# Performance work log

Hardware: AMD Instinct MI355X
Metric: run time of the kernel (lower is better)

The kernel has to match this reference:

```python
import jax, jax.numpy as jnp
import numpy as np
from jax import lax

NPOINT = 1024
K = 32
EPS = 1e-5  # BatchNorm eps (torch default)


def farthest_point_sample(xyz, npoint):
    # xyz: [B, N, 3] -> [B, npoint] int32 indices.
    # Deterministic variant: initial farthest point fixed to index 0
    # (original uses torch.randint; fixed seed point for reproducibility).
    B, N, _ = xyz.shape

    def step(carry, _):
        distance, farthest = carry  # [B,N], [B]
        centroid = jnp.take_along_axis(xyz, farthest[:, None, None], axis=1)  # [B,1,3]
        d = jnp.sum((xyz - centroid) ** 2, axis=-1)  # [B,N]
        distance = jnp.minimum(distance, d)
        new_far = jnp.argmax(distance, axis=-1).astype(jnp.int32)
        return (distance, new_far), farthest

    init = (jnp.full((B, N), 1e10, dtype=xyz.dtype), jnp.zeros((B,), jnp.int32))
    _, cents = lax.scan(step, init, None, length=npoint)  # [npoint, B]
    return cents.T  # [B, npoint]


def _gather_points(p, i):
    # p: [N, C], i: [S, K] -> [S, K, C]
    return p[i]


gather = jax.vmap(_gather_points)


def _mlp_layer(x, W, b, g, bt):
    # x: [B, Cin, K, S]; 1x1 Conv2d + BatchNorm2d (training stats) + ReLU
    y = jnp.einsum('bckn,oc->bokn', x, W) + b[None, :, None, None]
    m = y.mean(axis=(0, 2, 3), keepdims=True)
    v = y.var(axis=(0, 2, 3), keepdims=True)  # biased var, as torch BN training
    y = g[None, :, None, None] * (y - m) * lax.rsqrt(v + EPS) + bt[None, :, None, None]
    return jax.nn.relu(y)


def setup_inputs() -> dict:
    key = jax.random.key(0)
    ks = jax.random.split(key, 10)
    B, N, D = 16, 4096, 64
    xyz = jax.random.normal(ks[0], (B, N, 3), dtype=jnp.float32)
    points = jax.random.normal(ks[1], (B, N, D), dtype=jnp.float32)
    cin = 3 + D
    mlp = [64, 64, 128]
    params = {}
    last = cin
    for li, cout in enumerate(mlp):
        kw = jax.random.fold_in(ks[2], li)
        params[f'W{li+1}'] = jax.random.normal(kw, (cout, last), dtype=jnp.float32) * (1.0 / np.sqrt(last))
        params[f'b{li+1}'] = jnp.zeros((cout,), jnp.float32)
        params[f'g{li+1}'] = jnp.ones((cout,), jnp.float32)
        params[f'bt{li+1}'] = jnp.zeros((cout,), jnp.float32)
        last = cout
    return {'xyz': xyz, 'points': points, **params}


def reference(xyz, points, W1, b1, g1, bt1, W2, b2, g2, bt2, W3, b3, g3, bt3):
    # --- sample_and_group ---
    fidx = farthest_point_sample(xyz, NPOINT)                       # [B,S]
    new_xyz = jnp.take_along_axis(xyz, fidx[:, :, None], axis=1)    # [B,S,3]
    # pairwise squared distance centroids -> all points: [B,S,N]
    dist = jnp.sum((new_xyz[:, :, None, :] - xyz[:, None, :, :]) ** 2, axis=-1)
    _, idx = lax.top_k(-dist, K)                                    # k nearest, [B,S,K]
    grouped_xyz = gather(xyz, idx)                                  # [B,S,K,3]
    grouped_xyz_norm = grouped_xyz - new_xyz[:, :, None, :]
    grouped_pts = gather(points, idx)                               # [B,S,K,D]
    new_points = jnp.concatenate([grouped_xyz_norm, grouped_pts], axis=-1)  # [B,S,K,C]
    # --- pointwise MLP + max pool over neighbors ---
    x = jnp.transpose(new_points, (0, 3, 2, 1))                     # [B,C,K,S]
    x = _mlp_layer(x, W1, b1, g1, bt1)
    x = _mlp_layer(x, W2, b2, g2, bt2)
    x = _mlp_layer(x, W3, b3, g3, bt3)
    out = jnp.max(x, axis=2)                                        # [B,128,S]
    return (new_xyz, out)
```

## Files before the change

### kernel.cpp

```cpp
#include <hip/hip_runtime.h>
#include <hip/hip_bf16.h>

typedef __attribute__((ext_vector_type(8))) unsigned short u16x8;
typedef __attribute__((ext_vector_type(8))) short bf16x8;
typedef __attribute__((ext_vector_type(4))) float f32x4;

#define DEVI __device__ __forceinline__

constexpr int Bc = 16;
constexpr int Nc = 4096;
constexpr int Sc = 1024;
constexpr int Kc = 32;
constexpr int Dc = 64;
constexpr int C1 = 67;
constexpr int Mtot = Bc * Sc * Kc;
constexpr float EPSc = 1e-5f;
constexpr float CNTinv = 1.0f / (float)Mtot;
constexpr int NREP = 8;
constexpr int REPSTRIDE = 512;

DEVI float sqdist3(float dx, float dy, float dz) {
  return __fadd_rn(__fadd_rn(__fmul_rn(dx, dx), __fmul_rn(dy, dy)), __fmul_rn(dz, dz));
}
DEVI unsigned long long umax64(unsigned long long a, unsigned long long b) { return a > b ? a : b; }
DEVI float bf2f(unsigned short u) { return __uint_as_float(((unsigned)u) << 16); }
DEVI unsigned short f2bf(float f) {
  __hip_bfloat16 h = __float2bfloat16(f);
  unsigned short u;
  __builtin_memcpy(&u, &h, 2);
  return u;
}
DEVI unsigned pack_bf2(float a, float b) {
  return (unsigned)f2bf(a) | ((unsigned)f2bf(b) << 16);
}

#define DPP_STAGE(v, OP, CTRL, MASK)                                                       \
  {                                                                                        \
    int _t = __builtin_amdgcn_update_dpp(__float_as_int(v), __float_as_int(v), CTRL, MASK, \
                                         0xF, false);                                      \
    v = OP(v, __int_as_float(_t));                                                         \
  }
DEVI float wave_fmax63(float v) {
  DPP_STAGE(v, fmaxf, 0xB1, 0xF)
  DPP_STAGE(v, fmaxf, 0x4E, 0xF)
  DPP_STAGE(v, fmaxf, 0x141, 0xF)
  DPP_STAGE(v, fmaxf, 0x140, 0xF)
  DPP_STAGE(v, fmaxf, 0x142, 0xA)
  DPP_STAGE(v, fmaxf, 0x143, 0xC)
  return __int_as_float(__builtin_amdgcn_readlane(__float_as_int(v), 63));
}
DEVI float wave_fmin63(float v) {
  DPP_STAGE(v, fminf, 0xB1, 0xF)
  DPP_STAGE(v, fminf, 0x4E, 0xF)
  DPP_STAGE(v, fminf, 0x141, 0xF)
  DPP_STAGE(v, fminf, 0x140, 0xF)
  DPP_STAGE(v, fminf, 0x142, 0xA)
  DPP_STAGE(v, fminf, 0x143, 0xC)
  return __int_as_float(__builtin_amdgcn_readlane(__float_as_int(v), 63));
}
#define DPP_STAGE_U(v, CTRL, MASK)                                                      \
  {                                                                                     \
    unsigned _t = (unsigned)__builtin_amdgcn_update_dpp((int)(v), (int)(v), CTRL, MASK, \
                                                        0xF, false);                    \
    v = (_t < v) ? _t : v;                                                              \
  }
DEVI unsigned wave_umin63(unsigned v) {
  DPP_STAGE_U(v, 0xB1, 0xF)
  DPP_STAGE_U(v, 0x4E, 0xF)
  DPP_STAGE_U(v, 0x141, 0xF)
  DPP_STAGE_U(v, 0x140, 0xF)
  DPP_STAGE_U(v, 0x142, 0xA)
  DPP_STAGE_U(v, 0x143, 0xC)
  return (unsigned)__builtin_amdgcn_readlane((int)v, 63);
}

__global__ __launch_bounds__(256) void fps_kernel(const float* __restrict__ xyz,
                                                  int* __restrict__ fidx) {
  __shared__ float4 lsc[Nc];
  __shared__ __align__(16) unsigned long long wkey[2][4];
  __shared__ int sidx[Sc];
  const int b = blockIdx.x;
  const float* xb = xyz + (size_t)b * Nc * 3;
  const int tid = threadIdx.x;
  const int lane = tid & 63, w = tid >> 6;

  float px[16], py[16], pz[16], dist[16];
#pragma unroll
  for (int i = 0; i < 16; ++i) {
    int p = tid + i * 256;
    px[i] = xb[p * 3 + 0];
    py[i] = xb[p * 3 + 1];
    pz[i] = xb[p * 3 + 2];
    dist[i] = 1e10f;
  }
  for (int e = tid; e < Nc; e += 256)
    lsc[e] = make_float4(xb[e * 3 + 0], xb[e * 3 + 1], xb[e * 3 + 2], 0.f);
  if (tid == 0) sidx[0] = 0;
  __syncthreads();

  int widx = 0;
  for (int t = 1; t < Sc; ++t) {
    const float4 c = lsc[widx];
    float nd[16];
#pragma unroll
    for (int i = 0; i < 16; ++i) {
      float d = sqdist3(px[i] - c.x, py[i] - c.y, pz[i] - c.z);
      float v = fminf(dist[i], d);
      dist[i] = v;
      nd[i] = v;
    }
    float t8[8], t4[4];
#pragma unroll
    for (int u = 0; u < 8; ++u) t8[u] = fmaxf(nd[u], nd[u + 8]);
#pragma unroll
    for (int u = 0; u < 4; ++u) t4[u] = fmaxf(t8[u], t8[u + 4]);
    const float mymax = fmaxf(fmaxf(t4[0], t4[1]), fmaxf(t4[2], t4[3]));
    const float maxw = wave_fmax63(mymax);
    unsigned lp = 0xFFFFFFFFu;
#pragma unroll
    for (int i = 15; i >= 0; --i) lp = (nd[i] == maxw) ? (unsigned)(tid + (i << 8)) : lp;
    const unsigned long long mask = __ballot(mymax == maxw);
    unsigned wavep;
    if (__builtin_popcountll(mask) == 1) {
      wavep = (unsigned)__builtin_amdgcn_readlane((int)lp, (int)__builtin_ctzll(mask));
    } else {
      wavep = wave_umin63(lp);
    }
    if (lane == 0)
      wkey[t & 1][w] = ((unsigned long long)__float_as_uint(maxw) << 32) |
                       (unsigned long long)(0xFFFFFFFFu - wavep);
    __syncthreads();
    const ulonglong2* wp = (const ulonglong2*)wkey[t & 1];
    ulonglong2 a0 = wp[0], a1 = wp[1];
    unsigned long long m = umax64(umax64(a0.x, a0.y), umax64(a1.x, a1.y));
    widx = (int)(0xFFFFFFFFu - (unsigned)(m & 0xFFFFFFFFu));
    if (tid == 0) sidx[t] = widx;
  }
  __syncthreads();
  for (int e = tid; e < Sc; e += 256) fidx[b * Sc + e] = sidx[e];
}

__global__ __launch_bounds__(256) void knn_kernel(const float* __restrict__ xyz,
                                                  const int* __restrict__ fidx,
                                                  float* __restrict__ new_xyz,
                                                  int* __restrict__ idx) {
  const int w = threadIdx.x >> 6;
  const int lane = threadIdx.x & 63;
  const int q = blockIdx.x * 4 + w;
  const int b = q >> 10;
  const int s = q & (Sc - 1);
  const float* xb = xyz + (size_t)b * Nc * 3;
  const int ci = fidx[b * Sc + s];
  const float cx = xb[ci * 3 + 0], cy = xb[ci * 3 + 1], cz = xb[ci * 3 + 2];
  if (lane == 0) {
    new_xyz[(b * Sc + s) * 3 + 0] = cx;
    new_xyz[(b * Sc + s) * 3 + 1] = cy;
    new_xyz[(b * Sc + s) * 3 + 2] = cz;
  }
  const float INF = __int_as_float(0x7F800000);
  const float* pp = xb + lane * 3;
  float d0 = INF, d1 = INF;
  int i0 = 0, i1 = 0;
#pragma unroll 4
  for (int i = 0; i < 64; ++i) {
    const float x = pp[i * 192 + 0], y = pp[i * 192 + 1], z = pp[i * 192 + 2];
    const float d = sqdist3(x - cx, y - cy, z - cz);
    const bool c0 = d < d0, c1 = d < d1;
    d1 = c0 ? d0 : (c1 ? d : d1);
    i1 = c0 ? i0 : (c1 ? i : i1);
    d0 = c0 ? d : d0;
    i0 = c0 ? i : i0;
  }
  unsigned long long taken = 0ull;
  int* outp = idx + ((size_t)b * Sc + s) * Kc;
#pragma unroll 1
  for (int r = 0; r < Kc; ++r) {
    const float mind = wave_fmin63(d0);
    const unsigned myp = (unsigned)(lane + (i0 << 6));
    const unsigned long long mask = __ballot(d0 == mind);
    unsigned W;
    if (__builtin_popcountll(mask) == 1) {
      W = (unsigned)__builtin_amdgcn_readlane((int)myp, (int)__builtin_ctzll(mask));
    } else {
      unsigned c = (d0 == mind) ? myp : 0xFFFFFFFFu;
      W = wave_umin63(c);
    }
    if (lane == 0) outp[r] = (int)W;
    if (myp == W) {
      taken |= (1ull << i0);
      d0 = d1;
      i0 = i1;
      d1 = INF;
      if (__float_as_uint(d0) == 0x7F800000u) {
        float e0 = INF, e1 = INF;
        int j0 = 0, j1 = 0;
#pragma unroll 4
        for (int i = 0; i < 64; ++i) {
          const float x = pp[i * 192 + 0], y = pp[i * 192 + 1], z = pp[i * 192 + 2];
          float d = sqdist3(x - cx, y - cy, z - cz);
          d = ((taken >> i) & 1ull) ? INF : d;
          const bool c0b = d < e0, c1b = d < e1;
          e1 = c0b ? e0 : (c1b ? d : e1);
          j1 = c0b ? j0 : (c1b ? i : j1);
          e0 = c0b ? d : e0;
          j0 = c0b ? i : j0;
        }
        d0 = e0; i0 = j0; d1 = e1; i1 = j1;
      }
    }
  }
}

__global__ __launch_bounds__(256) void conv1_kernel(
    const float* __restrict__ xyz, const float* __restrict__ points,
    const float* __restrict__ new_xyz, const int* __restrict__ idx,
    const float* __restrict__ W1, const float* __restrict__ b1,
    __hip_bfloat16* __restrict__ x1, float* __restrict__ statsOut) {
  __shared__ float feats[C1][68];
  __shared__ float Wt[C1][64];
  __shared__ float red1[4][16][8];
  const int tid = threadIdx.x;
  const int lane = tid & 63, w = tid >> 6;
  const int m0 = blockIdx.x * 64;
  for (int e = tid; e < 64 * C1; e += 256) {
    int c = e / C1, j = e % C1;
    Wt[j][c] = W1[e];
  }
  {
    const int p = tid >> 2, qd = tid & 3;
    const int m = m0 + p;
    const int b = m >> 15;
    const int s = (m >> 5) & (Sc - 1);
    const int i = idx[m];
    const float* pr = points + ((size_t)b * Nc + i) * Dc + qd * 16;
    float4 v0 = *(const float4*)(pr + 0);
    float4 v1 = *(const float4*)(pr + 4);
    float4 v2 = *(const float4*)(pr + 8);
    float4 v3 = *(const float4*)(pr + 12);
    float vv[16] = {v0.x, v0.y, v0.z, v0.w, v1.x, v1.y, v1.z, v1.w,
                    v2.x, v2.y, v2.z, v2.w, v3.x, v3.y, v3.z, v3.w};
    const int j0 = 3 + qd * 16;
#pragma unroll
    for (int u = 0; u < 16; ++u) feats[j0 + u][p] = vv[u];
    if (qd == 0) {
      const float* xp = xyz + ((size_t)b * Nc + i) * 3;
      const float* cp = new_xyz + ((size_t)b * Sc + s) * 3;
      feats[0][p] = xp[0] - cp[0];
      feats[1][p] = xp[1] - cp[1];
      feats[2][p] = xp[2] - cp[2];
    }
  }
  __syncthreads();
  const int c0 = (tid & 15) * 4, p0 = (tid >> 4) * 4;
  float acc[4][4];
#pragma unroll
  for (int cc = 0; cc < 4; ++cc) {
    float bb = b1[c0 + cc];
#pragma unroll
    for (int pp = 0; pp < 4; ++pp) acc[pp][cc] = bb;
  }
#pragma unroll 4
  for (int j = 0; j < C1; ++j) {
    const float4 f = *(const float4*)&feats[j][p0];
    const float4 wv = *(const float4*)&Wt[j][c0];
    const float fa[4] = {f.x, f.y, f.z, f.w};
    const float wa[4] = {wv.x, wv.y, wv.z, wv.w};
#pragma unroll
    for (int pp = 0; pp < 4; ++pp)
#pragma unroll
      for (int cc = 0; cc < 4; ++cc) acc[pp][cc] = fmaf(fa[pp], wa[cc], acc[pp][cc]);
  }
  float s_[4] = {0.f, 0.f, 0.f, 0.f}, q_[4] = {0.f, 0.f, 0.f, 0.f};
#pragma unroll
  for (int pp = 0; pp < 4; ++pp) {
    unsigned short hv[4];
#pragma unroll
    for (int cc = 0; cc < 4; ++cc) {
      hv[cc] = f2bf(acc[pp][cc]);
      float fr = bf2f(hv[cc]);
      s_[cc] += fr;
      q_[cc] += fr * fr;
    }
    unsigned r0 = (unsigned)hv[0] | ((unsigned)hv[1] << 16);
    unsigned r1 = (unsigned)hv[2] | ((unsigned)hv[3] << 16);
    unsigned short* dst = (unsigned short*)x1 + (size_t)(m0 + p0 + pp) * 64 + c0;
    *(uint2*)dst = make_uint2(r0, r1);
  }
#pragma unroll
  for (int cc = 0; cc < 4; ++cc) {
    s_[cc] += __shfl_xor(s_[cc], 16, 64);
    s_[cc] += __shfl_xor(s_[cc], 32, 64);
    q_[cc] += __shfl_xor(q_[cc], 16, 64);
    q_[cc] += __shfl_xor(q_[cc], 32, 64);
  }
  if (lane < 16) {
#pragma unroll
    for (int cc = 0; cc < 4; ++cc) {
      red1[w][lane][cc] = s_[cc];
      red1[w][lane][4 + cc] = q_[cc];
    }
  }
  __syncthreads();
  if (tid < 128) {
    int h = tid >> 6, ch = tid & 63;
    int g = ch >> 2, cc = ch & 3;
    float v = red1[0][g][h * 4 + cc] + red1[1][g][h * 4 + cc] + red1[2][g][h * 4 + cc] +
              red1[3][g][h * 4 + cc];
    atomicAdd(&statsOut[(blockIdx.x & (NREP - 1)) * REPSTRIDE + h * 64 + ch], v);
  }
}

template <int COUT, bool LAST>
__global__ __launch_bounds__(256) void convm_kernel(
    const __hip_bfloat16* __restrict__ xin, const float* __restrict__ statsIn,
    const float* __restrict__ gamma, const float* __restrict__ beta,
    const float* __restrict__ W, const float* __restrict__ bias,
    float* __restrict__ statsOut, __hip_bfloat16* __restrict__ xout,
    unsigned* __restrict__ ymm) {
  constexpr int NT = COUT / 16;
  __shared__ __align__(16) unsigned short fA[64 * 64];
  __shared__ __align__(16) unsigned short fW[COUT * 64];
  __shared__ float scs[64], shs[64];
  __shared__ float red[4][COUT][2];
  __shared__ float redmm[LAST ? 4 : 1][COUT][2];
  __shared__ unsigned short fStage[64][72];
  const int tid = threadIdx.x;
  const int lane = tid & 63, w = tid >> 6;
  const long m0 = (long)blockIdx.x * 64;

  if (tid < 64) {
    float s0 = 0.f, s1 = 0.f;
#pragma unroll
    for (int r = 0; r < NREP; ++r) {
      s0 += statsIn[r * REPSTRIDE + tid];
      s1 += statsIn[r * REPSTRIDE + 64 + tid];
    }
    float mean = s0 * CNTinv;
    float var = s1 * CNTinv - mean * mean;
    float sc = gamma[tid] * rsqrtf(var + EPSc);
    scs[tid] = sc;
    shs[tid] = beta[tid] - mean * sc;
  }
  for (int e = tid; e < COUT * 64; e += 256) {
    int r = e >> 6, k = e & 63;
    int byte = (k * 2) ^ ((r & 7) << 4);
    fW[r * 64 + (byte >> 1)] = f2bf(W[e]);
  }
  __syncthreads();
  {
    const int row = tid >> 2, cb = tid & 3;
    const unsigned short* src = (const unsigned short*)xin + (m0 + row) * 64 + cb * 16;
    u16x8 a = *(const u16x8*)src;
    u16x8 bv = *(const u16x8*)(src + 8);
    unsigned short o[16];
#pragma unroll
    for (int u = 0; u < 8; ++u) {
      int ch = cb * 16 + u;
      o[u] = f2bf(fmaxf(fmaf(scs[ch], bf2f(a[u]), shs[ch]), 0.f));
    }
#pragma unroll
    for (int u = 0; u < 8; ++u) {
      int ch = cb * 16 + 8 + u;
      o[8 + u] = f2bf(fmaxf(fmaf(scs[ch], bf2f(bv[u]), shs[ch]), 0.f));
    }
    int sw = (row & 7) << 4;
    *(bf16x8*)((char*)fA + row * 128 + ((cb * 32) ^ sw)) = *(bf16x8*)&o[0];
    *(bf16x8*)((char*)fA + row * 128 + ((cb * 32 + 16) ^ sw)) = *(bf16x8*)&o[8];
  }
  __syncthreads();

  const int fr = lane & 15, kchunk = lane >> 4;
  f32x4 acc[NT];
#pragma unroll
  for (int nt = 0; nt < NT; ++nt) {
    float bb = bias[nt * 16 + fr];
    acc[nt] = f32x4{bb, bb, bb, bb};
  }
  bf16x8 af0, af1;
  {
    int row = w * 16 + fr;
    int sw = (row & 7) << 4;
    af0 = *(bf16x8*)((char*)fA + row * 128 + ((kchunk * 16) ^ sw));
    af1 = *(bf16x8*)((char*)fA + row * 128 + ((64 + kchunk * 16) ^ sw));
  }
#pragma unroll
  for (int nt = 0; nt < NT; ++nt) {
    int r2 = nt * 16 + fr;
    int sw = (r2 & 7) << 4;
    bf16x8 bf0 = *(bf16x8*)((char*)fW + r2 * 128 + ((kchunk * 16) ^ sw));
    bf16x8 bf1 = *(bf16x8*)((char*)fW + r2 * 128 + ((64 + kchunk * 16) ^ sw));
    acc[nt] = __builtin_amdgcn_mfma_f32_16x16x32_bf16(af0, bf0, acc[nt], 0, 0, 0);
    acc[nt] = __builtin_amdgcn_mfma_f32_16x16x32_bf16(af1, bf1, acc[nt], 0, 0, 0);
  }

  float s_[NT], q_[NT], mn_[NT], mx_[NT];
#pragma unroll
  for (int nt = 0; nt < NT; ++nt) {
    s_[nt] = 0.f;
    q_[nt] = 0.f;
    mn_[nt] = 1e30f;
    mx_[nt] = -1e30f;
    unsigned short hv[4];
#pragma unroll
    for (int r = 0; r < 4; ++r) {
      hv[r] = f2bf(acc[nt][r]);
      float fr2 = bf2f(hv[r]);
      s_[nt] += fr2;
      q_[nt] += fr2 * fr2;
      if constexpr (LAST) {
        mn_[nt] = fminf(mn_[nt], fr2);
        mx_[nt] = fmaxf(mx_[nt], fr2);
      }
    }
    if constexpr (!LAST) {
#pragma unroll
      for (int r = 0; r < 4; ++r) fStage[w * 16 + kchunk * 4 + r][nt * 16 + fr] = hv[r];
    }
  }
#pragma unroll
  for (int nt = 0; nt < NT; ++nt) {
    s_[nt] += __shfl_xor(s_[nt], 16, 64);
    s_[nt] += __shfl_xor(s_[nt], 32, 64);
    q_[nt] += __shfl_xor(q_[nt], 16, 64);
    q_[nt] += __shfl_xor(q_[nt], 32, 64);
    if constexpr (LAST) {
      mn_[nt] = fminf(mn_[nt], __shfl_xor(mn_[nt], 16, 64));
      mn_[nt] = fminf(mn_[nt], __shfl_xor(mn_[nt], 32, 64));
      mx_[nt] = fmaxf(mx_[nt], __shfl_xor(mx_[nt], 16, 64));
      mx_[nt] = fmaxf(mx_[nt], __shfl_xor(mx_[nt], 32, 64));
    }
  }
  if (lane < 16) {
#pragma unroll
    for (int nt = 0; nt < NT; ++nt) {
      red[w][nt * 16 + lane][0] = s_[nt];
      red[w][nt * 16 + lane][1] = q_[nt];
      if constexpr (LAST) {
        redmm[w][nt * 16 + lane][0] = mn_[nt];
        redmm[w][nt * 16 + lane][1] = mx_[nt];
      }
    }
  }
  __syncthreads();
  if (tid < 2 * COUT) {
    int ch = tid >> 1, h = tid & 1;
    float v = red[0][ch][h] + red[1][ch][h] + red[2][ch][h] + red[3][ch][h];
    atomicAdd(&statsOut[(blockIdx.x & (NREP - 1)) * REPSTRIDE + h * COUT + ch], v);
  }
  if constexpr (LAST) {
    int sg = tid >> 7, ch = tid & 127;
    float mn = fminf(redmm[sg * 2][ch][0], redmm[sg * 2 + 1][ch][0]);
    float mx = fmaxf(redmm[sg * 2][ch][1], redmm[sg * 2 + 1][ch][1]);
    ymm[(size_t)(m0 / 32 + sg) * 128 + ch] = pack_bf2(mn, mx);
  } else {
    int row = tid >> 2, cb = tid & 3;
    unsigned short* dst = (unsigned short*)xout + (m0 + row) * 64 + cb * 16;
    *(uint4*)dst = *(uint4*)&fStage[row][cb * 16];
    *(uint4*)(dst + 8) = *(uint4*)&fStage[row][cb * 16 + 8];
  }
}

__global__ __launch_bounds__(256) void pool_kernel(const unsigned* __restrict__ ymm,
                                                   const float* __restrict__ stats,
                                                   const float* __restrict__ gamma,
                                                   const float* __restrict__ beta,
                                                   float* __restrict__ out) {
  __shared__ float sc[128], sh[128];
  __shared__ float res[128][33];
  const int tid = threadIdx.x;
  if (tid < 128) {
    float s0 = 0.f, s1 = 0.f;
#pragma unroll
    for (int r = 0; r < NREP; ++r) {
      s0 += stats[r * REPSTRIDE + tid];
      s1 += stats[r * REPSTRIDE + 128 + tid];
    }
    float mean = s0 * CNTinv;
    float var = s1 * CNTinv - mean * mean;
    float s = gamma[tid] * rsqrtf(var + EPSc);
    sc[tid] = s;
    sh[tid] = beta[tid] - mean * s;
  }
  __syncthreads();
  const int b = blockIdx.x >> 5;
  const int s0 = (blockIdx.x & 31) * 32;
  const int w = tid >> 6, lane = tid & 63;
  const int c0 = lane * 2;
  const float sc0 = sc[c0], sh0 = sh[c0], sc1 = sc[c0 + 1], sh1 = sh[c0 + 1];
  for (int si = 0; si < 8; ++si) {
    const int s = s0 + w * 8 + si;
    uint2 v = *(const uint2*)&ymm[(size_t)(b * Sc + s) * 128 + c0];
    float f0 = (sc0 >= 0.f) ? bf2f((unsigned short)(v.x >> 16)) : bf2f((unsigned short)(v.x & 0xFFFFu));
    float f1 = (sc1 >= 0.f) ? bf2f((unsigned short)(v.y >> 16)) : bf2f((unsigned short)(v.y & 0xFFFFu));
    res[c0][s - s0] = fmaxf(fmaf(sc0, f0, sh0), 0.f);
    res[c0 + 1][s - s0] = fmaxf(fmaf(sc1, f1, sh1), 0.f);
  }
  __syncthreads();
  const int c = tid >> 1, h = tid & 1;
  float* ob = out + (size_t)b * 128 * Sc + (size_t)c * Sc + s0 + h * 16;
#pragma unroll
  for (int u = 0; u < 16; ++u) ob[u] = res[c][h * 16 + u];
}

extern "C" void kernel_launch(void* const* d_in, const int* in_sizes, int n_in,
                              void* d_out, int out_size, void* d_ws, size_t ws_size,
                              hipStream_t stream) {
  const float* xyz = (const float*)d_in[0];
  const float* points = (const float*)d_in[1];
  const float* W1 = (const float*)d_in[2];
  const float* b1 = (const float*)d_in[3];
  const float* g1 = (const float*)d_in[4];
  const float* bt1 = (const float*)d_in[5];
  const float* W2 = (const float*)d_in[6];
  const float* b2 = (const float*)d_in[7];
  const float* g2 = (const float*)d_in[8];
  const float* bt2 = (const float*)d_in[9];
  const float* W3 = (const float*)d_in[10];
  const float* b3 = (const float*)d_in[11];
  const float* g3 = (const float*)d_in[12];
  const float* bt3 = (const float*)d_in[13];
  float* out = (float*)d_out;

  char* ws = (char*)d_ws;
  int* fidx = (int*)(ws + 0);
  int* idx = (int*)(ws + 65536);
  float* stats = (float*)(ws + 2162688);
  __hip_bfloat16* x1 = (__hip_bfloat16*)(ws + 2162688 + 16384);
  __hip_bfloat16* x2 = (__hip_bfloat16*)(ws + 2162688 + 16384 + 67108864);
  unsigned* ymm = (unsigned*)(ws + 2162688 + 16384 + 134217728);

  hipMemsetAsync(stats, 0, NREP * REPSTRIDE * sizeof(float), stream);
  fps_kernel<<<Bc, 256, 0, stream>>>(xyz, fidx);
  knn_kernel<<<Bc * Sc / 4, 256, 0, stream>>>(xyz, fidx, out, idx);
  conv1_kernel<<<Mtot / 64, 256, 0, stream>>>(xyz, points, out, idx, W1, b1, x1, stats);
  convm_kernel<64, false><<<Mtot / 64, 256, 0, stream>>>(x1, stats, g1, bt1, W2, b2,
                                                         stats + 128, x2, nullptr);
  convm_kernel<128, true><<<Mtot / 64, 256, 0, stream>>>(x2, stats + 128, g2, bt2, W3, b3,
                                                         stats + 256, nullptr, ymm);
  pool_kernel<<<Bc * (Sc / 32), 256, 0, stream>>>(ymm, stats + 256, g3, bt3,
                                                  out + Bc * Sc * 3);
}
```

Before: 1.168 ms.

## Use packed 64-bit key argmax in FPS and keep top-4 per lane in KNN

In the farthest-point-sampling loop, each point's distance and inverted index are packed into one 64-bit key, so a single max reduction (per thread, then a DPP wave reduction on lo/hi halves) replaces the float max, ballot, tie-break min and readlane sequence. This shortens the serial per-iteration dependency chain at the cost of more 64-bit compares. In the KNN kernel, each lane now keeps its 4 nearest candidates instead of 2, so the costly rescan of its 64 points is needed less often during the 32 extraction rounds. The price is more select instructions per point and more registers.

```diff
diff --git a/kernel.cpp b/kernel.cpp
--- a/kernel.cpp
+++ b/kernel.cpp
@@ -40,15 +40,6 @@
                                          0xF, false);                                      \
     v = OP(v, __int_as_float(_t));                                                         \
   }
-DEVI float wave_fmax63(float v) {
-  DPP_STAGE(v, fmaxf, 0xB1, 0xF)
-  DPP_STAGE(v, fmaxf, 0x4E, 0xF)
-  DPP_STAGE(v, fmaxf, 0x141, 0xF)
-  DPP_STAGE(v, fmaxf, 0x140, 0xF)
-  DPP_STAGE(v, fmaxf, 0x142, 0xA)
-  DPP_STAGE(v, fmaxf, 0x143, 0xC)
-  return __int_as_float(__builtin_amdgcn_readlane(__float_as_int(v), 63));
-}
 DEVI float wave_fmin63(float v) {
   DPP_STAGE(v, fminf, 0xB1, 0xF)
   DPP_STAGE(v, fminf, 0x4E, 0xF)
@@ -72,6 +63,26 @@
   DPP_STAGE_U(v, 0x142, 0xA)
   DPP_STAGE_U(v, 0x143, 0xC)
   return (unsigned)__builtin_amdgcn_readlane((int)v, 63);
+}
+#define DPP_STAGE_U64(lo, hi, CTRL, MASK)                                                    \
+  {                                                                                          \
+    unsigned _olo = (unsigned)__builtin_amdgcn_update_dpp((int)(lo), (int)(lo), CTRL, MASK,  \
+                                                          0xF, false);                       \
+    unsigned _ohi = (unsigned)__builtin_amdgcn_update_dpp((int)(hi), (int)(hi), CTRL, MASK,  \
+                                                          0xF, false);                       \
+    bool _g = (_ohi > (hi)) || (_ohi == (hi) && _olo > (lo));                                \
+    lo = _g ? _olo : (lo);                                                                   \
+    hi = _g ? _ohi : (hi);                                                                   \
+  }
+DEVI void wave_umax64_63(unsigned& lo, unsigned& hi) {
+  DPP_STAGE_U64(lo, hi, 0xB1, 0xF)
+  DPP_STAGE_U64(lo, hi, 0x4E, 0xF)
+  DPP_STAGE_U64(lo, hi, 0x141, 0xF)
+  DPP_STAGE_U64(lo, hi, 0x140, 0xF)
+  DPP_STAGE_U64(lo, hi, 0x142, 0xA)
+  DPP_STAGE_U64(lo, hi, 0x143, 0xC)
+  lo = (unsigned)__builtin_amdgcn_readlane((int)lo, 63);
+  hi = (unsigned)__builtin_amdgcn_readlane((int)hi, 63);
 }
 
 __global__ __launch_bounds__(256) void fps_kernel(const float* __restrict__ xyz,
@@ -85,6 +96,7 @@
   const int lane = tid & 63, w = tid >> 6;
 
   float px[16], py[16], pz[16], dist[16];
+  unsigned comp[16];
 #pragma unroll
   for (int i = 0; i < 16; ++i) {
     int p = tid + i * 256;
@@ -92,6 +104,7 @@
     py[i] = xb[p * 3 + 1];
     pz[i] = xb[p * 3 + 2];
     dist[i] = 1e10f;
+    comp[i] = 0xFFFFFFFFu - (unsigned)p;
   }
   for (int e = tid; e < Nc; e += 256)
     lsc[e] = make_float4(xb[e * 3 + 0], xb[e * 3 + 1], xb[e * 3 + 2], 0.f);
@@ -101,34 +114,23 @@
   int widx = 0;
   for (int t = 1; t < Sc; ++t) {
     const float4 c = lsc[widx];
-    float nd[16];
+    unsigned long long k[16];
 #pragma unroll
     for (int i = 0; i < 16; ++i) {
       float d = sqdist3(px[i] - c.x, py[i] - c.y, pz[i] - c.z);
       float v = fminf(dist[i], d);
       dist[i] = v;
-      nd[i] = v;
-    }
-    float t8[8], t4[4];
-#pragma unroll
-    for (int u = 0; u < 8; ++u) t8[u] = fmaxf(nd[u], nd[u + 8]);
-#pragma unroll
-    for (int u = 0; u < 4; ++u) t4[u] = fmaxf(t8[u], t8[u + 4]);
-    const float mymax = fmaxf(fmaxf(t4[0], t4[1]), fmaxf(t4[2], t4[3]));
-    const float maxw = wave_fmax63(mymax);
-    unsigned lp = 0xFFFFFFFFu;
-#pragma unroll
-    for (int i = 15; i >= 0; --i) lp = (nd[i] == maxw) ? (unsigned)(tid + (i << 8)) : lp;
-    const unsigned long long mask = __ballot(mymax == maxw);
-    unsigned wavep;
-    if (__builtin_popcountll(mask) == 1) {
-      wavep = (unsigned)__builtin_amdgcn_readlane((int)lp, (int)__builtin_ctzll(mask));
-    } else {
-      wavep = wave_umin63(lp);
-    }
-    if (lane == 0)
-      wkey[t & 1][w] = ((unsigned long long)__float_as_uint(maxw) << 32) |
-                       (unsigned long long)(0xFFFFFFFFu - wavep);
+      k[i] = ((unsigned long long)__float_as_uint(v) << 32) | comp[i];
+    }
+    unsigned long long t8[8], t4[4];
+#pragma unroll
+    for (int u = 0; u < 8; ++u) t8[u] = umax64(k[u], k[u + 8]);
+#pragma unroll
+    for (int u = 0; u < 4; ++u) t4[u] = umax64(t8[u], t8[u + 4]);
+    unsigned long long mykey = umax64(umax64(t4[0], t4[1]), umax64(t4[2], t4[3]));
+    unsigned lo = (unsigned)mykey, hi = (unsigned)(mykey >> 32);
+    wave_umax64_63(lo, hi);
+    if (lane == 0) wkey[t & 1][w] = ((unsigned long long)hi << 32) | lo;
     __syncthreads();
     const ulonglong2* wp = (const ulonglong2*)wkey[t & 1];
     ulonglong2 a0 = wp[0], a1 = wp[1];
@@ -159,13 +161,17 @@
   }
   const float INF = __int_as_float(0x7F800000);
   const float* pp = xb + lane * 3;
-  float d0 = INF, d1 = INF;
-  int i0 = 0, i1 = 0;
+  float d0 = INF, d1 = INF, d2 = INF, d3 = INF;
+  int i0 = 0, i1 = 0, i2 = 0, i3 = 0;
 #pragma unroll 4
   for (int i = 0; i < 64; ++i) {
     const float x = pp[i * 192 + 0], y = pp[i * 192 + 1], z = pp[i * 192 + 2];
     const float d = sqdist3(x - cx, y - cy, z - cz);
-    const bool c0 = d < d0, c1 = d < d1;
+    const bool c0 = d < d0, c1 = d < d1, c2 = d < d2, c3 = d < d3;
+    d3 = c2 ? d2 : (c3 ? d : d3);
+    i3 = c2 ? i2 : (c3 ? i : i3);
+    d2 = c1 ? d1 : (c2 ? d : d2);
+    i2 = c1 ? i1 : (c2 ? i : i2);
     d1 = c0 ? d0 : (c1 ? d : d1);
     i1 = c0 ? i0 : (c1 ? i : i1);
     d0 = c0 ? d : d0;
@@ -188,24 +194,29 @@
     if (lane == 0) outp[r] = (int)W;
     if (myp == W) {
       taken |= (1ull << i0);
-      d0 = d1;
-      i0 = i1;
-      d1 = INF;
+      d0 = d1; i0 = i1;
+      d1 = d2; i1 = i2;
+      d2 = d3; i2 = i3;
+      d3 = INF;
       if (__float_as_uint(d0) == 0x7F800000u) {
-        float e0 = INF, e1 = INF;
-        int j0 = 0, j1 = 0;
+        float e0 = INF, e1 = INF, e2 = INF, e3 = INF;
+        int j0 = 0, j1 = 0, j2 = 0, j3 = 0;
 #pragma unroll 4
         for (int i = 0; i < 64; ++i) {
           const float x = pp[i * 192 + 0], y = pp[i * 192 + 1], z = pp[i * 192 + 2];
           float d = sqdist3(x - cx, y - cy, z - cz);
           d = ((taken >> i) & 1ull) ? INF : d;
-          const bool c0b = d < e0, c1b = d < e1;
+          const bool c0b = d < e0, c1b = d < e1, c2b = d < e2, c3b = d < e3;
+          e3 = c2b ? e2 : (c3b ? d : e3);
+          j3 = c2b ? j2 : (c3b ? i : j3);
+          e2 = c1b ? e1 : (c2b ? d : e2);
+          j2 = c1b ? j1 : (c2b ? i : j2);
           e1 = c0b ? e0 : (c1b ? d : e1);
           j1 = c0b ? j0 : (c1b ? i : j1);
           e0 = c0b ? d : e0;
           j0 = c0b ? i : j0;
         }
-        d0 = e0; i0 = j0; d1 = e1; i1 = j1;
+        d0 = e0; i0 = j0; d1 = e1; i1 = j1; d2 = e2; i2 = j2; d3 = e3; i3 = j3;
       }
     }
   }
```

Measured after the change: 1.025 ms. 1.14x faster.

## Fuse FPS, kNN and conv1 into one persistent kernel with flag-based dataflow

Applied to the files above, without the earlier changes.

Merges the three kernels into a single launch whose block ranges act as FPS, kNN and conv1 workers. FPS publishes centroid indices in batches of eight through atomics, kNN waves spin until their centroid appears, and conv1 blocks wait on per-query done flags, so kNN and conv1 can run while FPS is still going. It also widens the per-lane kNN candidate list from two to four entries, which cuts down rescans, and stores FPS coordinates as separate arrays instead of float4. The cost is spin-wait polling and a larger shared-memory union. Forward progress relies on FPS blocks being scheduled before the waiting blocks, which low block IDs make likely but do not guarantee.

```diff
diff --git a/kernel.cpp b/kernel.cpp
--- a/kernel.cpp
+++ b/kernel.cpp
@@ -18,6 +18,9 @@
 constexpr float CNTinv = 1.0f / (float)Mtot;
 constexpr int NREP = 8;
 constexpr int REPSTRIDE = 512;
+constexpr int NB_FPS = Bc;
+constexpr int NB_KNN = Bc * Sc / 4;
+constexpr int NB_CONV = Mtot / 64;
 
 DEVI float sqdist3(float dx, float dy, float dz) {
   return __fadd_rn(__fadd_rn(__fmul_rn(dx, dx), __fmul_rn(dy, dy)), __fmul_rn(dz, dz));
@@ -74,239 +77,276 @@
   return (unsigned)__builtin_amdgcn_readlane((int)v, 63);
 }
 
-__global__ __launch_bounds__(256) void fps_kernel(const float* __restrict__ xyz,
-                                                  int* __restrict__ fidx) {
-  __shared__ float4 lsc[Nc];
-  __shared__ __align__(16) unsigned long long wkey[2][4];
-  __shared__ int sidx[Sc];
-  const int b = blockIdx.x;
-  const float* xb = xyz + (size_t)b * Nc * 3;
+struct FpsS {
+  float lsx[Nc], lsy[Nc], lsz[Nc];
+  int sidx[Sc];
+  unsigned long long wkey[2][4];
+};
+struct ConvS {
+  float feats[C1][68];
+  float Wt[C1][64];
+  float red1[4][16][8];
+};
+union SmemU {
+  FpsS f;
+  ConvS c;
+};
+
+__global__ __launch_bounds__(256) void mega_kernel(
+    const float* __restrict__ xyz, const float* __restrict__ points,
+    const float* __restrict__ W1, const float* __restrict__ b1,
+    int* fidx, int* idx, int* qdone, float* statsOut,
+    __hip_bfloat16* __restrict__ x1, float* out) {
+  __shared__ SmemU sm;
+  const int bid = blockIdx.x;
   const int tid = threadIdx.x;
   const int lane = tid & 63, w = tid >> 6;
 
-  float px[16], py[16], pz[16], dist[16];
-#pragma unroll
-  for (int i = 0; i < 16; ++i) {
-    int p = tid + i * 256;
-    px[i] = xb[p * 3 + 0];
-    py[i] = xb[p * 3 + 1];
-    pz[i] = xb[p * 3 + 2];
-    dist[i] = 1e10f;
-  }
-  for (int e = tid; e < Nc; e += 256)
-    lsc[e] = make_float4(xb[e * 3 + 0], xb[e * 3 + 1], xb[e * 3 + 2], 0.f);
-  if (tid == 0) sidx[0] = 0;
-  __syncthreads();
-
-  int widx = 0;
-  for (int t = 1; t < Sc; ++t) {
-    const float4 c = lsc[widx];
-    float nd[16];
+  if (bid < NB_FPS) {
+    const int b = bid;
+    const float* xb = xyz + (size_t)b * Nc * 3;
+    float px[16], py[16], pz[16], dist[16];
 #pragma unroll
     for (int i = 0; i < 16; ++i) {
-      float d = sqdist3(px[i] - c.x, py[i] - c.y, pz[i] - c.z);
-      float v = fminf(dist[i], d);
-      dist[i] = v;
-      nd[i] = v;
-    }
-    float t8[8], t4[4];
-#pragma unroll
-    for (int u = 0; u < 8; ++u) t8[u] = fmaxf(nd[u], nd[u + 8]);
-#pragma unroll
-    for (int u = 0; u < 4; ++u) t4[u] = fmaxf(t8[u], t8[u + 4]);
-    const float mymax = fmaxf(fmaxf(t4[0], t4[1]), fmaxf(t4[2], t4[3]));
-    const float maxw = wave_fmax63(mymax);
-    unsigned lp = 0xFFFFFFFFu;
-#pragma unroll
-    for (int i = 15; i >= 0; --i) lp = (nd[i] == maxw) ? (unsigned)(tid + (i << 8)) : lp;
-    const unsigned long long mask = __ballot(mymax == maxw);
-    unsigned wavep;
-    if (__builtin_popcountll(mask) == 1) {
-      wavep = (unsigned)__builtin_amdgcn_readlane((int)lp, (int)__builtin_ctzll(mask));
-    } else {
-      wavep = wave_umin63(lp);
-    }
-    if (lane == 0)
-      wkey[t & 1][w] = ((unsigned long long)__float_as_uint(maxw) << 32) |
-                       (unsigned long long)(0xFFFFFFFFu - wavep);
+      int p = tid + i * 256;
+      px[i] = xb[p * 3 + 0];
+      py[i] = xb[p * 3 + 1];
+      pz[i] = xb[p * 3 + 2];
+      dist[i] = 1e10f;
+    }
+    for (int e = tid; e < Nc; e += 256) {
+      sm.f.lsx[e] = xb[e * 3 + 0];
+      sm.f.lsy[e] = xb[e * 3 + 1];
+      sm.f.lsz[e] = xb[e * 3 + 2];
+    }
+    if (tid == 0) atomicExch(&fidx[b * Sc], 0);
     __syncthreads();
-    const ulonglong2* wp = (const ulonglong2*)wkey[t & 1];
-    ulonglong2 a0 = wp[0], a1 = wp[1];
-    unsigned long long m = umax64(umax64(a0.x, a0.y), umax64(a1.x, a1.y));
-    widx = (int)(0xFFFFFFFFu - (unsigned)(m & 0xFFFFFFFFu));
-    if (tid == 0) sidx[t] = widx;
-  }
-  __syncthreads();
-  for (int e = tid; e < Sc; e += 256) fidx[b * Sc + e] = sidx[e];
-}
-
-__global__ __launch_bounds__(256) void knn_kernel(const float* __restrict__ xyz,
-                                                  const int* __restrict__ fidx,
-                                                  float* __restrict__ new_xyz,
-                                                  int* __restrict__ idx) {
-  const int w = threadIdx.x >> 6;
-  const int lane = threadIdx.x & 63;
-  const int q = blockIdx.x * 4 + w;
-  const int b = q >> 10;
-  const int s = q & (Sc - 1);
-  const float* xb = xyz + (size_t)b * Nc * 3;
-  const int ci = fidx[b * Sc + s];
-  const float cx = xb[ci * 3 + 0], cy = xb[ci * 3 + 1], cz = xb[ci * 3 + 2];
-  if (lane == 0) {
-    new_xyz[(b * Sc + s) * 3 + 0] = cx;
-    new_xyz[(b * Sc + s) * 3 + 1] = cy;
-    new_xyz[(b * Sc + s) * 3 + 2] = cz;
-  }
-  const float INF = __int_as_float(0x7F800000);
-  const float* pp = xb + lane * 3;
-  float d0 = INF, d1 = INF;
-  int i0 = 0, i1 = 0;
+
+    int widx = 0;
+    for (int t = 1; t < Sc; ++t) {
+      const float cx = sm.f.lsx[widx], cy = sm.f.lsy[widx], cz = sm.f.lsz[widx];
+      float nd[16];
+#pragma unroll
+      for (int i = 0; i < 16; ++i) {
+        float d = sqdist3(px[i] - cx, py[i] - cy, pz[i] - cz);
+        float v = fminf(dist[i], d);
+        dist[i] = v;
+        nd[i] = v;
+      }
+      float t8[8], t4[4];
+#pragma unroll
+      for (int u = 0; u < 8; ++u) t8[u] = fmaxf(nd[u], nd[u + 8]);
+#pragma unroll
+      for (int u = 0; u < 4; ++u) t4[u] = fmaxf(t8[u], t8[u + 4]);
+      const float mymax = fmaxf(fmaxf(t4[0], t4[1]), fmaxf(t4[2], t4[3]));
+      const float maxw = wave_fmax63(mymax);
+      unsigned lp = 0xFFFFFFFFu;
+#pragma unroll
+      for (int i = 15; i >= 0; --i) lp = (nd[i] == maxw) ? (unsigned)(tid + (i << 8)) : lp;
+      const unsigned long long mask = __ballot(mymax == maxw);
+      unsigned wavep;
+      if (__builtin_popcountll(mask) == 1) {
+        wavep = (unsigned)__builtin_amdgcn_readlane((int)lp, (int)__builtin_ctzll(mask));
+      } else {
+        wavep = wave_umin63(lp);
+      }
+      if (lane == 0)
+        sm.f.wkey[t & 1][w] = ((unsigned long long)__float_as_uint(maxw) << 32) |
+                              (unsigned long long)(0xFFFFFFFFu - wavep);
+      __syncthreads();
+      const ulonglong2* wp = (const ulonglong2*)sm.f.wkey[t & 1];
+      ulonglong2 a0 = wp[0], a1 = wp[1];
+      unsigned long long m = umax64(umax64(a0.x, a0.y), umax64(a1.x, a1.y));
+      widx = (int)(0xFFFFFFFFu - (unsigned)(m & 0xFFFFFFFFu));
+      if (tid == 0) {
+        sm.f.sidx[t] = widx;
+        if ((t & 7) == 0 || t == Sc - 1) {
+          int base = t - ((t - 1) & 7);
+          for (int u = base; u <= t; ++u) atomicExch(&fidx[b * Sc + u], sm.f.sidx[u]);
+        }
+      }
+    }
+    return;
+  }
+
+  if (bid < NB_FPS + NB_KNN) {
+    const int q = (bid - NB_FPS) * 4 + w;
+    const int b = q >> 10;
+    const int s = q & (Sc - 1);
+    const float* xb = xyz + (size_t)b * Nc * 3;
+    int ci = -1;
+    if (lane == 0) {
+      while ((ci = atomicAdd(&fidx[b * Sc + s], 0)) < 0) __builtin_amdgcn_s_sleep(16);
+    }
+    ci = __shfl(ci, 0, 64);
+    const float cx = xb[ci * 3 + 0], cy = xb[ci * 3 + 1], cz = xb[ci * 3 + 2];
+    if (lane == 0) {
+      atomicExch(&out[(b * Sc + s) * 3 + 0], cx);
+      atomicExch(&out[(b * Sc + s) * 3 + 1], cy);
+      atomicExch(&out[(b * Sc + s) * 3 + 2], cz);
+    }
+    const float INF = __int_as_float(0x7F800000);
+    const float* pp = xb + lane * 3;
+    float d0 = INF, d1 = INF, d2 = INF, d3 = INF;
+    int i0 = 0, i1 = 0, i2 = 0, i3 = 0;
 #pragma unroll 4
-  for (int i = 0; i < 64; ++i) {
-    const float x = pp[i * 192 + 0], y = pp[i * 192 + 1], z = pp[i * 192 + 2];
-    const float d = sqdist3(x - cx, y - cy, z - cz);
-    const bool c0 = d < d0, c1 = d < d1;
-    d1 = c0 ? d0 : (c1 ? d : d1);
-    i1 = c0 ? i0 : (c1 ? i : i1);
-    d0 = c0 ? d : d0;
-    i0 = c0 ? i : i0;
-  }
-  unsigned long long taken = 0ull;
-  int* outp = idx + ((size_t)b * Sc + s) * Kc;
+    for (int i = 0; i < 64; ++i) {
+      const float x = pp[i * 192 + 0], y = pp[i * 192 + 1], z = pp[i * 192 + 2];
+      const float d = sqdist3(x - cx, y - cy, z - cz);
+      const bool c0 = d < d0, c1 = d < d1, c2 = d < d2, c3 = d < d3;
+      d3 = c2 ? d2 : (c3 ? d : d3);
+      i3 = c2 ? i2 : (c3 ? i : i3);
+      d2 = c1 ? d1 : (c2 ? d : d2);
+      i2 = c1 ? i1 : (c2 ? i : i2);
+      d1 = c0 ? d0 : (c1 ? d : d1);
+      i1 = c0 ? i0 : (c1 ? i : i1);
+      d0 = c0 ? d : d0;
+      i0 = c0 ? i : i0;
+    }
+    unsigned long long taken = 0ull;
+    int* outp = idx + ((size_t)b * Sc + s) * Kc;
 #pragma unroll 1
-  for (int r = 0; r < Kc; ++r) {
-    const float mind = wave_fmin63(d0);
-    const unsigned myp = (unsigned)(lane + (i0 << 6));
-    const unsigned long long mask = __ballot(d0 == mind);
-    unsigned W;
-    if (__builtin_popcountll(mask) == 1) {
-      W = (unsigned)__builtin_amdgcn_readlane((int)myp, (int)__builtin_ctzll(mask));
-    } else {
-      unsigned c = (d0 == mind) ? myp : 0xFFFFFFFFu;
-      W = wave_umin63(c);
-    }
-    if (lane == 0) outp[r] = (int)W;
-    if (myp == W) {
-      taken |= (1ull << i0);
-      d0 = d1;
-      i0 = i1;
-      d1 = INF;
-      if (__float_as_uint(d0) == 0x7F800000u) {
-        float e0 = INF, e1 = INF;
-        int j0 = 0, j1 = 0;
+    for (int r = 0; r < Kc; ++r) {
+      const float mind = wave_fmin63(d0);
+      const unsigned myp = (unsigned)(lane + (i0 << 6));
+      const unsigned long long mask = __ballot(d0 == mind);
+      unsigned W;
+      if (__builtin_popcountll(mask) == 1) {
+        W = (unsigned)__builtin_amdgcn_readlane((int)myp, (int)__builtin_ctzll(mask));
+      } else {
+        unsigned c = (d0 == mind) ? myp : 0xFFFFFFFFu;
+        W = wave_umin63(c);
+      }
+      if (lane == 0) atomicExch(&outp[r], (int)W);
+      if (myp == W) {
+        taken |= (1ull << i0);
+        d0 = d1; i0 = i1;
+        d1 = d2; i1 = i2;
+        d2 = d3; i2 = i3;
+        d3 = INF;
+        if (__float_as_uint(d0) == 0x7F800000u) {
+          float e0 = INF, e1 = INF, e2 = INF, e3 = INF;
+          int j0 = 0, j1 = 0, j2 = 0, j3 = 0;
 #pragma unroll 4
-        for (int i = 0; i < 64; ++i) {
-          const float x = pp[i * 192 + 0], y = pp[i * 192 + 1], z = pp[i * 192 + 2];
-          float d = sqdist3(x - cx, y - cy, z - cz);
-          d = ((taken >> i) & 1ull) ? INF : d;
-          const bool c0b = d < e0, c1b = d < e1;
-          e1 = c0b ? e0 : (c1b ? d : e1);
-          j1 = c0b ? j0 : (c1b ? i : j1);
-          e0 = c0b ? d : e0;
-          j0 = c0b ? i : j0;
+          for (int i = 0; i < 64; ++i) {
+            const float x = pp[i * 192 + 0], y = pp[i * 192 + 1], z = pp[i * 192 + 2];
+            float d = sqdist3(x - cx, y - cy, z - cz);
+            d = ((taken >> i) & 1ull) ? INF : d;
+            const bool c0b = d < e0, c1b = d < e1, c2b = d < e2, c3b = d < e3;
+            e3 = c2b ? e2 : (c3b ? d : e3);
+            j3 = c2b ? j2 : (c3b ? i : j3);
+            e2 = c1b ? e1 : (c2b ? d : e2);
+            j2 = c1b ? j1 : (c2b ? i : j2);
+            e1 = c0b ? e0 : (c1b ? d : e1);
+            j1 = c0b ? j0 : (c1b ? i : j1);
+            e0 = c0b ? d : e0;
+            j0 = c0b ? i : j0;
+          }
+          d0 = e0; i0 = j0; d1 = e1; i1 = j1; d2 = e2; i2 = j2; d3 = e3; i3 = j3;
         }
-        d0 = e0; i0 = j0; d1 = e1; i1 = j1;
-      }
-    }
-  }
-}
-
-__global__ __launch_bounds__(256) void conv1_kernel(
-    const float* __restrict__ xyz, const float* __restrict__ points,
-    const float* __restrict__ new_xyz, const int* __restrict__ idx,
-    const float* __restrict__ W1, const float* __restrict__ b1,
-    __hip_bfloat16* __restrict__ x1, float* __restrict__ statsOut) {
-  __shared__ float feats[C1][68];
-  __shared__ float Wt[C1][64];
-  __shared__ float red1[4][16][8];
-  const int tid = threadIdx.x;
-  const int lane = tid & 63, w = tid >> 6;
-  const int m0 = blockIdx.x * 64;
-  for (int e = tid; e < 64 * C1; e += 256) {
-    int c = e / C1, j = e % C1;
-    Wt[j][c] = W1[e];
-  }
+      }
+    }
+    if (lane == 0) {
+      __threadfence();
+      atomicExch(&qdone[q], 1);
+    }
+    return;
+  }
+
   {
-    const int p = tid >> 2, qd = tid & 3;
-    const int m = m0 + p;
-    const int b = m >> 15;
-    const int s = (m >> 5) & (Sc - 1);
-    const int i = idx[m];
-    const float* pr = points + ((size_t)b * Nc + i) * Dc + qd * 16;
-    float4 v0 = *(const float4*)(pr + 0);
-    float4 v1 = *(const float4*)(pr + 4);
-    float4 v2 = *(const float4*)(pr + 8);
-    float4 v3 = *(const float4*)(pr + 12);
-    float vv[16] = {v0.x, v0.y, v0.z, v0.w, v1.x, v1.y, v1.z, v1.w,
-                    v2.x, v2.y, v2.z, v2.w, v3.x, v3.y, v3.z, v3.w};
-    const int j0 = 3 + qd * 16;
-#pragma unroll
-    for (int u = 0; u < 16; ++u) feats[j0 + u][p] = vv[u];
-    if (qd == 0) {
-      const float* xp = xyz + ((size_t)b * Nc + i) * 3;
-      const float* cp = new_xyz + ((size_t)b * Sc + s) * 3;
-      feats[0][p] = xp[0] - cp[0];
-      feats[1][p] = xp[1] - cp[1];
-      feats[2][p] = xp[2] - cp[2];
-    }
-  }
-  __syncthreads();
-  const int c0 = (tid & 15) * 4, p0 = (tid >> 4) * 4;
-  float acc[4][4];
-#pragma unroll
-  for (int cc = 0; cc < 4; ++cc) {
-    float bb = b1[c0 + cc];
-#pragma unroll
-    for (int pp = 0; pp < 4; ++pp) acc[pp][cc] = bb;
-  }
+    const int cb = bid - NB_FPS - NB_KNN;
+    const int m0 = cb * 64;
+    for (int e = tid; e < 64 * C1; e += 256) {
+      int c = e / C1, j = e % C1;
+      sm.c.Wt[j][c] = W1[e];
+    }
+    if (tid == 0 || tid == 64) {
+      const int qq = (cb << 1) + (tid >> 6);
+      while (atomicAdd(&qdone[qq], 0) == 0) __builtin_amdgcn_s_sleep(16);
+    }
+    __syncthreads();
+    {
+      const int p = tid >> 2, qd = tid & 3;
+      const int m = m0 + p;
+      const int b = m >> 15;
+      const int s = (m >> 5) & (Sc - 1);
+      const int i = idx[m];
+      const float* pr = points + ((size_t)b * Nc + i) * Dc + qd * 16;
+      float4 v0 = *(const float4*)(pr + 0);
+      float4 v1 = *(const float4*)(pr + 4);
+      float4 v2 = *(const float4*)(pr + 8);
+      float4 v3 = *(const float4*)(pr + 12);
+      float vv[16] = {v0.x, v0.y, v0.z, v0.w, v1.x, v1.y, v1.z, v1.w,
+                      v2.x, v2.y, v2.z, v2.w, v3.x, v3.y, v3.z, v3.w};
+      const int j0 = 3 + qd * 16;
+#pragma unroll
+      for (int u = 0; u < 16; ++u) sm.c.feats[j0 + u][p] = vv[u];
+      if (qd == 0) {
+        const float* xp = xyz + ((size_t)b * Nc + i) * 3;
+        const float* cp = out + ((size_t)b * Sc + s) * 3;
+        sm.c.feats[0][p] = xp[0] - cp[0];
+        sm.c.feats[1][p] = xp[1] - cp[1];
+        sm.c.feats[2][p] = xp[2] - cp[2];
+      }
+    }
+    __syncthreads();
+    const int c0 = (tid & 15) * 4, p0 = (tid >> 4) * 4;
+    float acc[4][4];
+#pragma unroll
+    for (int cc = 0; cc < 4; ++cc) {
+      float bb = b1[c0 + cc];
+#pragma unroll
+      for (int pp = 0; pp < 4; ++pp) acc[pp][cc] = bb;
+    }
 #pragma unroll 4
-  for (int j = 0; j < C1; ++j) {
-    const float4 f = *(const float4*)&feats[j][p0];
-    const float4 wv = *(const float4*)&Wt[j][c0];
-    const float fa[4] = {f.x, f.y, f.z, f.w};
-    const float wa[4] = {wv.x, wv.y, wv.z, wv.w};
-#pragma unroll
-    for (int pp = 0; pp < 4; ++pp)
-#pragma unroll
-      for (int cc = 0; cc < 4; ++cc) acc[pp][cc] = fmaf(fa[pp], wa[cc], acc[pp][cc]);
-  }
-  float s_[4] = {0.f, 0.f, 0.f, 0.f}, q_[4] = {0.f, 0.f, 0.f, 0.f};
-#pragma unroll
-  for (int pp = 0; pp < 4; ++pp) {
-    unsigned short hv[4];
+    for (int j = 0; j < C1; ++j) {
+      const float4 f = *(const float4*)&sm.c.feats[j][p0];
+      const float4 wv = *(const float4*)&sm.c.Wt[j][c0];
+      const float fa[4] = {f.x, f.y, f.z, f.w};
+      const float wa[4] = {wv.x, wv.y, wv.z, wv.w};
+#pragma unroll
+      for (int pp = 0; pp < 4; ++pp)
+#pragma unroll
+        for (int cc = 0; cc < 4; ++cc) acc[pp][cc] = fmaf(fa[pp], wa[cc], acc[pp][cc]);
+    }
+    float s_[4] = {0.f, 0.f, 0.f, 0.f}, q_[4] = {0.f, 0.f, 0.f, 0.f};
+#pragma unroll
+    for (int pp = 0; pp < 4; ++pp) {
+      unsigned short hv[4];
+#pragma unroll
+      for (int cc = 0; cc < 4; ++cc) {
+        hv[cc] = f2bf(acc[pp][cc]);
+        float fr = bf2f(hv[cc]);
+        s_[cc] += fr;
+        q_[cc] += fr * fr;
+      }
+      unsigned r0 = (unsigned)hv[0] | ((unsigned)hv[1] << 16);
+      unsigned r1 = (unsigned)hv[2] | ((unsigned)hv[3] << 16);
+      unsigned short* dst = (unsigned short*)x1 + (size_t)(m0 + p0 + pp) * 64 + c0;
+      *(uint2*)dst = make_uint2(r0, r1);
+    }
 #pragma unroll
     for (int cc = 0; cc < 4; ++cc) {
-      hv[cc] = f2bf(acc[pp][cc]);
-      float fr = bf2f(hv[cc]);
-      s_[cc] += fr;
-      q_[cc] += fr * fr;
-    }
-    unsigned r0 = (unsigned)hv[0] | ((unsigned)hv[1] << 16);
-    unsigned r1 = (unsigned)hv[2] | ((unsigned)hv[3] << 16);
-    unsigned short* dst = (unsigned short*)x1 + (size_t)(m0 + p0 + pp) * 64 + c0;
-    *(uint2*)dst = make_uint2(r0, r1);
-  }
-#pragma unroll
-  for (int cc = 0; cc < 4; ++cc) {
-    s_[cc] += __shfl_xor(s_[cc], 16, 64);
-    s_[cc] += __shfl_xor(s_[cc], 32, 64);
-    q_[cc] += __shfl_xor(q_[cc], 16, 64);
-    q_[cc] += __shfl_xor(q_[cc], 32, 64);
-  }
-  if (lane < 16) {
-#pragma unroll
-    for (int cc = 0; cc < 4; ++cc) {
-      red1[w][lane][cc] = s_[cc];
-      red1[w][lane][4 + cc] = q_[cc];
-    }
-  }
-  __syncthreads();
-  if (tid < 128) {
-    int h = tid >> 6, ch = tid & 63;
-    int g = ch >> 2, cc = ch & 3;
-    float v = red1[0][g][h * 4 + cc] + red1[1][g][h * 4 + cc] + red1[2][g][h * 4 + cc] +
-              red1[3][g][h * 4 + cc];
-    atomicAdd(&statsOut[(blockIdx.x & (NREP - 1)) * REPSTRIDE + h * 64 + ch], v);
+      s_[cc] += __shfl_xor(s_[cc], 16, 64);
+      s_[cc] += __shfl_xor(s_[cc], 32, 64);
+      q_[cc] += __shfl_xor(q_[cc], 16, 64);
+      q_[cc] += __shfl_xor(q_[cc], 32, 64);
+    }
+    if (lane < 16) {
+#pragma unroll
+      for (int cc = 0; cc < 4; ++cc) {
+        sm.c.red1[w][lane][cc] = s_[cc];
+        sm.c.red1[w][lane][4 + cc] = q_[cc];
+      }
+    }
+    __syncthreads();
+    if (tid < 128) {
+      int h = tid >> 6, ch = tid & 63;
+      int g = ch >> 2, cc = ch & 3;
+      float v = sm.c.red1[0][g][h * 4 + cc] + sm.c.red1[1][g][h * 4 + cc] +
+                sm.c.red1[2][g][h * 4 + cc] + sm.c.red1[3][g][h * 4 + cc];
+      atomicAdd(&statsOut[(cb & (NREP - 1)) * REPSTRIDE + h * 64 + ch], v);
+    }
   }
 }
 
@@ -445,7 +485,7 @@
   if (tid < 2 * COUT) {
     int ch = tid >> 1, h = tid & 1;
     float v = red[0][ch][h] + red[1][ch][h] + red[2][ch][h] + red[3][ch][h];
-    atomicAdd(&statsOut[(blockIdx.x & (NREP - 1)) * REPSTRIDE + h * COUT + ch], v);
+    atomicAdd(&statsOut[((int)blockIdx.x & (NREP - 1)) * REPSTRIDE + h * COUT + ch], v);
   }
   if constexpr (LAST) {
     int sg = tid >> 7, ch = tid & 127;
@@ -525,14 +565,16 @@
   int* fidx = (int*)(ws + 0);
   int* idx = (int*)(ws + 65536);
   float* stats = (float*)(ws + 2162688);
-  __hip_bfloat16* x1 = (__hip_bfloat16*)(ws + 2162688 + 16384);
-  __hip_bfloat16* x2 = (__hip_bfloat16*)(ws + 2162688 + 16384 + 67108864);
-  unsigned* ymm = (unsigned*)(ws + 2162688 + 16384 + 134217728);
+  int* qdone = (int*)(ws + 2179072);
+  __hip_bfloat16* x1 = (__hip_bfloat16*)(ws + 2244608);
+  __hip_bfloat16* x2 = (__hip_bfloat16*)(ws + 2244608 + 67108864);
+  unsigned* ymm = (unsigned*)(ws + 2244608 + 134217728);
 
   hipMemsetAsync(stats, 0, NREP * REPSTRIDE * sizeof(float), stream);
-  fps_kernel<<<Bc, 256, 0, stream>>>(xyz, fidx);
-  knn_kernel<<<Bc * Sc / 4, 256, 0, stream>>>(xyz, fidx, out, idx);
-  conv1_kernel<<<Mtot / 64, 256, 0, stream>>>(xyz, points, out, idx, W1, b1, x1, stats);
+  hipMemsetAsync(fidx, 0xFF, Bc * Sc * sizeof(int), stream);
+  hipMemsetAsync(qdone, 0, Bc * Sc * sizeof(int), stream);
+  mega_kernel<<<NB_FPS + NB_KNN + NB_CONV, 256, 0, stream>>>(xyz, points, W1, b1, fidx, idx,
+                                                             qdone, stats, x1, out);
   convm_kernel<64, false><<<Mtot / 64, 256, 0, stream>>>(x1, stats, g1, bt1, W2, b2,
                                                          stats + 128, x2, nullptr);
   convm_kernel<128, true><<<Mtot / 64, 256, 0, stream>>>(x2, stats + 128, g2, bt2, W3, b3,
```

After: 1.079 ms. 7.6% less time.
